# Optimization experiments

Measured on AMD Instinct MI355X. Metric: run time of the kernel, lower is better.

Reference implementation:

```python
import jax, jax.numpy as jnp
import numpy as np

NUM_LAYERS = 3
HIDDEN = 128
EDGE_CH = 4
VOCAB = 100
N_NODES = 100000
N_EDGES = 600000


def setup_inputs() -> dict:
    key = jax.random.key(0)
    ks = jax.random.split(key, 10)
    z = jax.random.randint(ks[0], (N_NODES,), 0, VOCAB)
    edge_index = jax.random.randint(ks[1], (2, N_EDGES), 0, N_NODES)
    edge_attr = jax.random.normal(ks[2], (N_EDGES, EDGE_CH), dtype=jnp.float32)
    batch_vec = jnp.sort(jax.random.randint(ks[3], (N_NODES,), 0, 512))
    s = 1.0 / np.sqrt(HIDDEN)
    emb = jax.random.normal(ks[4], (VOCAB, HIDDEN), dtype=jnp.float32)
    We = jax.random.normal(ks[5], (NUM_LAYERS, EDGE_CH, HIDDEN), dtype=jnp.float32) * 0.5
    be = jnp.zeros((NUM_LAYERS, HIDDEN), dtype=jnp.float32)
    W1 = jax.random.normal(ks[6], (NUM_LAYERS, HIDDEN, HIDDEN), dtype=jnp.float32) * s
    b1 = jnp.zeros((NUM_LAYERS, HIDDEN), dtype=jnp.float32)
    W2 = jax.random.normal(ks[7], (NUM_LAYERS, HIDDEN, HIDDEN), dtype=jnp.float32) * s
    b2 = jnp.zeros((NUM_LAYERS, HIDDEN), dtype=jnp.float32)
    return {"emb": emb, "We": We, "be": be, "W1": W1, "b1": b1,
            "W2": W2, "b2": b2, "edge_attr": edge_attr,
            "z": z, "edge_index": edge_index, "batch_vec": batch_vec}


def reference(emb, We, be, W1, b1, W2, b2, edge_attr, z, edge_index, batch_vec):
    # atom embedding lookup: [N, H]
    x = emb[z]
    src, dst = edge_index[0], edge_index[1]
    n = x.shape[0]
    for l in range(NUM_LAYERS):
        # edge feature projection: [E, H]
        e = edge_attr @ We[l] + be[l]
        # GINE message: relu(x_j + e_ij), gather over src nodes
        m = jax.nn.relu(x[src] + e)
        # scatter-sum aggregation to destination nodes
        agg = jax.ops.segment_sum(m, dst, num_segments=n)
        # (1 + eps) * x + agg, eps = 0, then 2-layer MLP with silu act
        h = x + agg
        x = jax.nn.silu(h @ W1[l] + b1[l]) @ W2[l] + b2[l]
    return (x, batch_vec)
```

## Files before the change

### kernel.cpp

```cpp
#include <hip/hip_runtime.h>
#include <hip/hip_fp16.h>
#include <math.h>

#define N_NODES 100000
#define N_EDGES 600000
#define HIDDEN 128
#define EDGE_CH 4
#define NUM_LAYERS 3
#define MLP_ROWS 64

#define SCAN_BLOCK 256
#define SCAN_GRID ((N_NODES + SCAN_BLOCK - 1) / SCAN_BLOCK)

#define HSTR 132
#define MLP3_TILES ((N_NODES + 127) / 128)
#define MLP3_GRID 256

#define EMB_BLOCKS ((N_NODES * 32) / 256)
#define ZB_BLOCKS  ((N_NODES + 255) / 256)
#define WP_BLOCKS  ((NUM_LAYERS * 2 * HIDDEN * HIDDEN) / 256)

typedef short bf16x8 __attribute__((ext_vector_type(8)));
typedef float f32x4  __attribute__((ext_vector_type(4)));

__device__ inline unsigned short f2bf(float x) {
    unsigned u = __float_as_uint(x);
    return (unsigned short)((u + 0x7fff + ((u >> 16) & 1)) >> 16);
}
__device__ inline float bf2f(unsigned short b) { return __uint_as_float(((unsigned)b) << 16); }

__device__ inline float4 h8tof4(uint2 u) {
    __half2 a = *reinterpret_cast<const __half2*>(&u.x);
    __half2 b = *reinterpret_cast<const __half2*>(&u.y);
    float2 fa = __half22float2(a);
    float2 fb = __half22float2(b);
    return make_float4(fa.x, fa.y, fb.x, fb.y);
}
__device__ inline uint2 f4toh8(float4 v) {
    __half2 a = __floats2half2_rn(v.x, v.y);
    __half2 b = __floats2half2_rn(v.z, v.w);
    uint2 u;
    u.x = *reinterpret_cast<unsigned*>(&a);
    u.y = *reinterpret_cast<unsigned*>(&b);
    return u;
}


__global__ void setup_kernel(const float* __restrict__ emb,
                             const int* __restrict__ z,
                             float* __restrict__ x,
                             __half* __restrict__ xh,
                             int write_xh, int write_x,
                             int* __restrict__ pos,
                             const int* __restrict__ bv,
                             float* __restrict__ out,
                             const float* __restrict__ W1,
                             const float* __restrict__ W2,
                             unsigned short* __restrict__ wt,
                             int do_wprep) {
    int b = blockIdx.x;
    if (b < EMB_BLOCKS) {
        int t = b * 256 + threadIdx.x;
        int node = t >> 5;
        int c4 = t & 31;
        if (node < N_NODES) {
            float4 v = ((const float4*)(emb + (size_t)z[node] * HIDDEN))[c4];
            if (write_x)
                ((float4*)(x + (size_t)node * HIDDEN))[c4] = v;
            if (write_xh)
                ((uint2*)(xh + (size_t)node * HIDDEN))[c4] = f4toh8(v);
        }
    } else if (b < EMB_BLOCKS + ZB_BLOCKS) {
        int i = (b - EMB_BLOCKS) * 256 + threadIdx.x;
        if (i < N_NODES) {
            pos[i] = 0;
            out[i] = (float)bv[i];
        }
    } else if (do_wprep) {
        int idx = (b - EMB_BLOCKS - ZB_BLOCKS) * 256 + threadIdx.x;
        if (idx < NUM_LAYERS * 2 * HIDDEN * HIDDEN) {
            int j    = idx & 7;
            int lane = (idx >> 3) & 63;
            int ks   = (idx >> 9) & 3;
            int nt   = (idx >> 11) & 7;
            int mat  = (idx >> 14) & 1;
            int l    = idx >> 15;
            int n = nt * 16 + (lane & 15);
            int k = ks * 32 + (lane >> 4) * 8 + j;
            const float* W = mat ? W2 : W1;
            wt[idx] = f2bf(W[(size_t)l * HIDDEN * HIDDEN + (size_t)k * HIDDEN + n]);
        }
    }
}


__global__ void embed_init_kernel(const float* __restrict__ emb,
                                  const int* __restrict__ z,
                                  float* __restrict__ x,
                                  float* __restrict__ agg,
                                  int write_agg,
                                  __half* __restrict__ xh,
                                  int write_xh,
                                  int write_x) {
    int t = blockIdx.x * blockDim.x + threadIdx.x;
    int node = t >> 5;
    int c4 = t & 31;
    if (node < N_NODES) {
        float4 v = ((const float4*)(emb + (size_t)z[node] * HIDDEN))[c4];
        if (write_x)
            ((float4*)(x + (size_t)node * HIDDEN))[c4] = v;
        if (write_agg)
            ((float4*)(agg + (size_t)node * HIDDEN))[c4] = v;
        if (write_xh)
            ((uint2*)(xh + (size_t)node * HIDDEN))[c4] = f4toh8(v);
    }
}

__global__ __launch_bounds__(512, 1) void mlp_mfma3_kernel(
        const void* __restrict__ hbuf,
        int h_half,
        const unsigned short* __restrict__ wfrag,
        const float* __restrict__ b1, const float* __restrict__ b2,
        float* __restrict__ x,
        __half* __restrict__ xh,
        int write_x, int write_xh) {
    __shared__ short wlds[2 * 16384];
    __shared__ float tbuf[8 * 16 * HSTR];
    int tid   = threadIdx.x;
    int wave  = tid >> 6;
    int lane  = tid & 63;
    int row16 = lane & 15;
    int quad  = lane >> 4;
    float* myt = tbuf + wave * 16 * HSTR;

    for (int i = tid; i < 4096; i += 512)
        ((float4*)wlds)[i] = ((const float4*)wfrag)[i];
    __syncthreads();

    float bias1[8], bias2[8];
    #pragma unroll
    for (int nt = 0; nt < 8; nt++) {
        bias1[nt] = b1[nt * 16 + row16];
        bias2[nt] = b2[nt * 16 + row16];
    }

    for (int tile = blockIdx.x; tile < MLP3_TILES; tile += gridDim.x) {
        int wnode0 = tile * 128 + wave * 16;
        int mnode  = wnode0 + row16;
        bool valid = (mnode < N_NODES);
        int srcnode = valid ? mnode : 0;

        bf16x8 ahi[4], alo[4];
        if (h_half) {
            const __half* hrow = (const __half*)hbuf + (size_t)srcnode * HIDDEN + quad * 8;
            #pragma unroll
            for (int ks = 0; ks < 4; ks++) {
                float v[8];
                if (valid) {
                    uint4 u = *(const uint4*)(hrow + ks * 32);
                    const __half2* hp = reinterpret_cast<const __half2*>(&u);
                    float2 f0 = __half22float2(hp[0]);
                    float2 f1 = __half22float2(hp[1]);
                    float2 f2 = __half22float2(hp[2]);
                    float2 f3 = __half22float2(hp[3]);
                    v[0]=f0.x; v[1]=f0.y; v[2]=f1.x; v[3]=f1.y;
                    v[4]=f2.x; v[5]=f2.y; v[6]=f3.x; v[7]=f3.y;
                } else {
                    #pragma unroll
                    for (int j = 0; j < 8; j++) v[j] = 0.f;
                }
                bf16x8 hi, lo;
                #pragma unroll
                for (int j = 0; j < 8; j++) {
                    unsigned short hb = f2bf(v[j]);
                    hi[j] = (short)hb;
                    lo[j] = (short)f2bf(v[j] - bf2f(hb));
                }
                ahi[ks] = hi; alo[ks] = lo;
            }
        } else {
            const float* hrow = (const float*)hbuf + (size_t)srcnode * HIDDEN + quad * 8;
            #pragma unroll
            for (int ks = 0; ks < 4; ks++) {
                float v[8];
                *(float4*)(v + 0) = valid ? *(const float4*)(hrow + ks * 32 + 0) : make_float4(0.f,0.f,0.f,0.f);
                *(float4*)(v + 4) = valid ? *(const float4*)(hrow + ks * 32 + 4) : make_float4(0.f,0.f,0.f,0.f);
                bf16x8 hi, lo;
                #pragma unroll
                for (int j = 0; j < 8; j++) {
                    unsigned short hb = f2bf(v[j]);
                    hi[j] = (short)hb;
                    lo[j] = (short)f2bf(v[j] - bf2f(hb));
                }
                ahi[ks] = hi; alo[ks] = lo;
            }
        }

        f32x4 acc[8];
        #pragma unroll
        for (int nt = 0; nt < 8; nt++) acc[nt] = (f32x4){0.f, 0.f, 0.f, 0.f};
        #pragma unroll
        for (int ks = 0; ks < 4; ks++) {
            #pragma unroll
            for (int nt = 0; nt < 8; nt++) {
                bf16x8 Bv = *(const bf16x8*)(wlds + (size_t)((nt * 4 + ks) * 64 + lane) * 8);
                acc[nt] = __builtin_amdgcn_mfma_f32_16x16x32_bf16(ahi[ks], Bv, acc[nt], 0, 0, 0);
                acc[nt] = __builtin_amdgcn_mfma_f32_16x16x32_bf16(alo[ks], Bv, acc[nt], 0, 0, 0);
            }
        }

        #pragma unroll
        for (int nt = 0; nt < 8; nt++) {
            #pragma unroll
            for (int r = 0; r < 4; r++) {
                float v = acc[nt][r] + bias1[nt];
                v = v / (1.f + __expf(-v));
                myt[(quad * 4 + r) * HSTR + nt * 16 + row16] = v;
            }
        }

        #pragma unroll
        for (int ks = 0; ks < 4; ks++) {
            const float* p = myt + row16 * HSTR + ks * 32 + quad * 8;
            float v[8];
            *(float4*)(v + 0) = *(const float4*)(p + 0);
            *(float4*)(v + 4) = *(const float4*)(p + 4);
            bf16x8 hi, lo;
            #pragma unroll
            for (int j = 0; j < 8; j++) {
                unsigned short hb = f2bf(v[j]);
                hi[j] = (short)hb;
                lo[j] = (short)f2bf(v[j] - bf2f(hb));
            }
            ahi[ks] = hi; alo[ks] = lo;
        }

        #pragma unroll
        for (int nt = 0; nt < 8; nt++) acc[nt] = (f32x4){0.f, 0.f, 0.f, 0.f};
        #pragma unroll
        for (int ks = 0; ks < 4; ks++) {
            #pragma unroll
            for (int nt = 0; nt < 8; nt++) {
                bf16x8 Bv = *(const bf16x8*)(wlds + (size_t)(16384 + ((nt * 4 + ks) * 64 + lane) * 8));
                acc[nt] = __builtin_amdgcn_mfma_f32_16x16x32_bf16(ahi[ks], Bv, acc[nt], 0, 0, 0);
                acc[nt] = __builtin_amdgcn_mfma_f32_16x16x32_bf16(alo[ks], Bv, acc[nt], 0, 0, 0);
            }
        }

        #pragma unroll
        for (int nt = 0; nt < 8; nt++) {
            #pragma unroll
            for (int r = 0; r < 4; r++)
                myt[(quad * 4 + r) * HSTR + nt * 16 + row16] = acc[nt][r] + bias2[nt];
        }
        int onode = wnode0 + row16;
        if (onode < N_NODES) {
            const float* prow = myt + row16 * HSTR + quad * 32;
            if (write_x) {
                float* orow = x + (size_t)onode * HIDDEN + quad * 32;
                #pragma unroll
                for (int j = 0; j < 8; j++)
                    *(float4*)(orow + 4 * j) = *(const float4*)(prow + 4 * j);
            }
            if (write_xh) {
                uint2* hrow2 = (uint2*)(xh + (size_t)onode * HIDDEN + quad * 32);
                #pragma unroll
                for (int j = 0; j < 8; j++)
                    hrow2[j] = f4toh8(*(const float4*)(prow + 4 * j));
            }
        }
    }
}

__global__ void mlp_kernel(const float* __restrict__ h,
                           const float* __restrict__ W1, const float* __restrict__ b1,
                           const float* __restrict__ W2, const float* __restrict__ b2,
                           float* __restrict__ x) {
    __shared__ float hs[MLP_ROWS * HIDDEN];
    int rg = threadIdx.x >> 5;
    int c4 = threadIdx.x & 31;
    int node0 = blockIdx.x * MLP_ROWS;

    for (int i = threadIdx.x; i < MLP_ROWS * 32; i += 256) {
        int node = node0 + (i >> 5);
        float4 v = (node < N_NODES)
                 ? ((const float4*)(h + (size_t)node * HIDDEN))[i & 31]
                 : make_float4(0.f, 0.f, 0.f, 0.f);
        ((float4*)hs)[i] = v;
    }
    __syncthreads();

    float4 acc[8];
    {
        float4 bv = ((const float4*)b1)[c4];
        #pragma unroll
        for (int r = 0; r < 8; r++) acc[r] = bv;
    }
    const float* hbase = hs + rg * 8 * HIDDEN;

    for (int k4 = 0; k4 < HIDDEN; k4 += 4) {
        float4 w0 = ((const float4*)(W1 + (size_t)(k4 + 0) * HIDDEN))[c4];
        float4 w1 = ((const float4*)(W1 + (size_t)(k4 + 1) * HIDDEN))[c4];
        float4 w2 = ((const float4*)(W1 + (size_t)(k4 + 2) * HIDDEN))[c4];
        float4 w3 = ((const float4*)(W1 + (size_t)(k4 + 3) * HIDDEN))[c4];
        #pragma unroll
        for (int r = 0; r < 8; r++) {
            float4 hv = *(const float4*)(hbase + r * HIDDEN + k4);
            acc[r].x += hv.x*w0.x + hv.y*w1.x + hv.z*w2.x + hv.w*w3.x;
            acc[r].y += hv.x*w0.y + hv.y*w1.y + hv.z*w2.y + hv.w*w3.y;
            acc[r].z += hv.x*w0.z + hv.y*w1.z + hv.z*w2.z + hv.w*w3.z;
            acc[r].w += hv.x*w0.w + hv.y*w1.w + hv.z*w2.w + hv.w*w3.w;
        }
    }

    __syncthreads();
    #pragma unroll
    for (int r = 0; r < 8; r++) {
        float4 a = acc[r];
        a.x = a.x / (1.f + __expf(-a.x));
        a.y = a.y / (1.f + __expf(-a.y));
        a.z = a.z / (1.f + __expf(-a.z));
        a.w = a.w / (1.f + __expf(-a.w));
        *(float4*)(hs + (rg * 8 + r) * HIDDEN + c4 * 4) = a;
    }
    __syncthreads();

    {
        float4 bv = ((const float4*)b2)[c4];
        #pragma unroll
        for (int r = 0; r < 8; r++) acc[r] = bv;
    }
    for (int k4 = 0; k4 < HIDDEN; k4 += 4) {
        float4 w0 = ((const float4*)(W2 + (size_t)(k4 + 0) * HIDDEN))[c4];
        float4 w1 = ((const float4*)(W2 + (size_t)(k4 + 1) * HIDDEN))[c4];
        float4 w2 = ((const float4*)(W2 + (size_t)(k4 + 2) * HIDDEN))[c4];
        float4 w3 = ((const float4*)(W2 + (size_t)(k4 + 3) * HIDDEN))[c4];
        #pragma unroll
        for (int r = 0; r < 8; r++) {
            float4 hv = *(const float4*)(hbase + r * HIDDEN + k4);
            acc[r].x += hv.x*w0.x + hv.y*w1.x + hv.z*w2.x + hv.w*w3.x;
            acc[r].y += hv.x*w0.y + hv.y*w1.y + hv.z*w2.y + hv.w*w3.y;
            acc[r].z += hv.x*w0.z + hv.y*w1.z + hv.z*w2.z + hv.w*w3.z;
            acc[r].w += hv.x*w0.w + hv.y*w1.w + hv.z*w2.w + hv.w*w3.w;
        }
    }

    #pragma unroll
    for (int r = 0; r < 8; r++) {
        int node = node0 + rg * 8 + r;
        if (node < N_NODES)
            ((float4*)(x + (size_t)node * HIDDEN))[c4] = acc[r];
    }
}

__global__ void batch_out_kernel(const int* __restrict__ bv, float* __restrict__ out) {
    int i = blockIdx.x * blockDim.x + threadIdx.x;
    if (i < N_NODES) out[i] = (float)bv[i];
}


__global__ void zero_kernel(int* __restrict__ p, int n) {
    int i = blockIdx.x * blockDim.x + threadIdx.x;
    if (i < n) p[i] = 0;
}

__global__ void hist_kernel(const int* __restrict__ dst, int* __restrict__ cnt) {
    int e = blockIdx.x * blockDim.x + threadIdx.x;
    if (e < N_EDGES) atomicAdd(&cnt[dst[e]], 1);
}

__global__ void scan_partial_kernel(const int* __restrict__ cnt, int* __restrict__ bsum) {
    __shared__ int s[SCAN_BLOCK];
    int i = blockIdx.x * SCAN_BLOCK + threadIdx.x;
    s[threadIdx.x] = (i < N_NODES) ? cnt[i] : 0;
    __syncthreads();
    for (int off = SCAN_BLOCK / 2; off > 0; off >>= 1) {
        if (threadIdx.x < off) s[threadIdx.x] += s[threadIdx.x + off];
        __syncthreads();
    }
    if (threadIdx.x == 0) bsum[blockIdx.x] = s[0];
}

__global__ void scan_base_kernel(int* __restrict__ bsum) {
    __shared__ int s[512];
    int t = threadIdx.x;
    s[t] = (t < SCAN_GRID) ? bsum[t] : 0;
    __syncthreads();
    for (int off = 1; off < 512; off <<= 1) {
        int v = (t >= off) ? s[t - off] : 0;
        __syncthreads();
        s[t] += v;
        __syncthreads();
    }
    if (t < SCAN_GRID) bsum[t] = (t > 0) ? s[t - 1] : 0;
}

__global__ void scan_final_kernel(int* __restrict__ cnt, const int* __restrict__ bsum) {
    __shared__ int s[SCAN_BLOCK];
    int i = blockIdx.x * SCAN_BLOCK + threadIdx.x;
    int v = (i < N_NODES) ? cnt[i] : 0;
    s[threadIdx.x] = v;
    __syncthreads();
    for (int off = 1; off < SCAN_BLOCK; off <<= 1) {
        int u = (threadIdx.x >= off) ? s[threadIdx.x - off] : 0;
        __syncthreads();
        s[threadIdx.x] += u;
        __syncthreads();
    }
    if (i < N_NODES) cnt[i] = bsum[blockIdx.x] + s[threadIdx.x] - v;
}

__global__ void scatter2_kernel(const int* __restrict__ dst,
                                const int* __restrict__ src,
                                const float* __restrict__ edge_attr,
                                int* __restrict__ pos,
                                int* __restrict__ ssrc,
                                float4* __restrict__ sea) {
    int e = blockIdx.x * blockDim.x + threadIdx.x;
    if (e < N_EDGES) {
        int p = atomicAdd(&pos[dst[e]], 1);
        ssrc[p] = src[e];
        sea[p] = ((const float4*)edge_attr)[e];
    }
}

__global__ void gather2_kernel(const float* __restrict__ x,
                               const int* __restrict__ ssrc,
                               const float4* __restrict__ sea,
                               const int* __restrict__ pos,
                               const float* __restrict__ We_l,
                               const float* __restrict__ be_l,
                               float* __restrict__ h) {
    __shared__ float sWe[EDGE_CH * HIDDEN];
    __shared__ float sbe[HIDDEN];
    for (int i = threadIdx.x; i < EDGE_CH * HIDDEN; i += blockDim.x) sWe[i] = We_l[i];
    if (threadIdx.x < HIDDEN) sbe[threadIdx.x] = be_l[threadIdx.x];
    __syncthreads();

    int t = blockIdx.x * blockDim.x + threadIdx.x;
    int node = t >> 5;
    int c4 = t & 31;
    if (node >= N_NODES) return;

    int start = (node == 0) ? 0 : pos[node - 1];
    int end = pos[node];

    float4 w0 = ((const float4*)sWe)[0 * 32 + c4];
    float4 w1 = ((const float4*)sWe)[1 * 32 + c4];
    float4 w2 = ((const float4*)sWe)[2 * 32 + c4];
    float4 w3 = ((const float4*)sWe)[3 * 32 + c4];
    float4 bb = ((const float4*)sbe)[c4];

    float4 acc = make_float4(0.f, 0.f, 0.f, 0.f);
    int j = start;
    if (j < end) {
        int s0 = ssrc[j];
        float4 ea0 = sea[j];
        for (; j + 1 < end; j++) {
            int s1 = ssrc[j + 1];
            float4 ea1 = sea[j + 1];
            float4 xv = ((const float4*)(x + (size_t)s0 * HIDDEN))[c4];
            float m0 = xv.x + ea0.x*w0.x + ea0.y*w1.x + ea0.z*w2.x + ea0.w*w3.x + bb.x;
            float m1 = xv.y + ea0.x*w0.y + ea0.y*w1.y + ea0.z*w2.y + ea0.w*w3.y + bb.y;
            float m2 = xv.z + ea0.x*w0.z + ea0.y*w1.z + ea0.z*w2.z + ea0.w*w3.z + bb.z;
            float m3 = xv.w + ea0.x*w0.w + ea0.y*w1.w + ea0.z*w2.w + ea0.w*w3.w + bb.w;
            acc.x += fmaxf(m0, 0.f); acc.y += fmaxf(m1, 0.f);
            acc.z += fmaxf(m2, 0.f); acc.w += fmaxf(m3, 0.f);
            s0 = s1; ea0 = ea1;
        }
        float4 xv = ((const float4*)(x + (size_t)s0 * HIDDEN))[c4];
        float m0 = xv.x + ea0.x*w0.x + ea0.y*w1.x + ea0.z*w2.x + ea0.w*w3.x + bb.x;
        float m1 = xv.y + ea0.x*w0.y + ea0.y*w1.y + ea0.z*w2.y + ea0.w*w3.y + bb.y;
        float m2 = xv.z + ea0.x*w0.z + ea0.y*w1.z + ea0.z*w2.z + ea0.w*w3.z + bb.z;
        float m3 = xv.w + ea0.x*w0.w + ea0.y*w1.w + ea0.z*w2.w + ea0.w*w3.w + bb.w;
        acc.x += fmaxf(m0, 0.f); acc.y += fmaxf(m1, 0.f);
        acc.z += fmaxf(m2, 0.f); acc.w += fmaxf(m3, 0.f);
    }
    float4 xi = ((const float4*)(x + (size_t)node * HIDDEN))[c4];
    acc.x += xi.x; acc.y += xi.y; acc.z += xi.z; acc.w += xi.w;
    ((float4*)(h + (size_t)node * HIDDEN))[c4] = acc;
}

__global__ void gather3_kernel(const __half* __restrict__ xh,
                               const int* __restrict__ ssrc,
                               const float4* __restrict__ sea,
                               const int* __restrict__ pos,
                               const float* __restrict__ We_l,
                               const float* __restrict__ be_l,
                               __half* __restrict__ h) {
    __shared__ float sWe[EDGE_CH * HIDDEN];
    __shared__ float sbe[HIDDEN];
    for (int i = threadIdx.x; i < EDGE_CH * HIDDEN; i += blockDim.x) sWe[i] = We_l[i];
    if (threadIdx.x < HIDDEN) sbe[threadIdx.x] = be_l[threadIdx.x];
    __syncthreads();

    int t = blockIdx.x * blockDim.x + threadIdx.x;
    int node = t >> 5;
    int c4 = t & 31;
    if (node >= N_NODES) return;

    int start = (node == 0) ? 0 : pos[node - 1];
    int end = pos[node];

    float4 w0 = ((const float4*)sWe)[0 * 32 + c4];
    float4 w1 = ((const float4*)sWe)[1 * 32 + c4];
    float4 w2 = ((const float4*)sWe)[2 * 32 + c4];
    float4 w3 = ((const float4*)sWe)[3 * 32 + c4];
    float4 bb = ((const float4*)sbe)[c4];

    float4 acc = make_float4(0.f, 0.f, 0.f, 0.f);
    int j = start;
    if (j < end) {
        int s0 = ssrc[j];
        float4 ea0 = sea[j];
        for (; j + 1 < end; j++) {
            int s1 = ssrc[j + 1];
            float4 ea1 = sea[j + 1];
            float4 xv = h8tof4(((const uint2*)(xh + (size_t)s0 * HIDDEN))[c4]);
            float m0 = xv.x + ea0.x*w0.x + ea0.y*w1.x + ea0.z*w2.x + ea0.w*w3.x + bb.x;
            float m1 = xv.y + ea0.x*w0.y + ea0.y*w1.y + ea0.z*w2.y + ea0.w*w3.y + bb.y;
            float m2 = xv.z + ea0.x*w0.z + ea0.y*w1.z + ea0.z*w2.z + ea0.w*w3.z + bb.z;
            float m3 = xv.w + ea0.x*w0.w + ea0.y*w1.w + ea0.z*w2.w + ea0.w*w3.w + bb.w;
            acc.x += fmaxf(m0, 0.f); acc.y += fmaxf(m1, 0.f);
            acc.z += fmaxf(m2, 0.f); acc.w += fmaxf(m3, 0.f);
            s0 = s1; ea0 = ea1;
        }
        float4 xv = h8tof4(((const uint2*)(xh + (size_t)s0 * HIDDEN))[c4]);
        float m0 = xv.x + ea0.x*w0.x + ea0.y*w1.x + ea0.z*w2.x + ea0.w*w3.x + bb.x;
        float m1 = xv.y + ea0.x*w0.y + ea0.y*w1.y + ea0.z*w2.y + ea0.w*w3.y + bb.y;
        float m2 = xv.z + ea0.x*w0.z + ea0.y*w1.z + ea0.z*w2.z + ea0.w*w3.z + bb.z;
        float m3 = xv.w + ea0.x*w0.w + ea0.y*w1.w + ea0.z*w2.w + ea0.w*w3.w + bb.w;
        acc.x += fmaxf(m0, 0.f); acc.y += fmaxf(m1, 0.f);
        acc.z += fmaxf(m2, 0.f); acc.w += fmaxf(m3, 0.f);
    }
    float4 xi = h8tof4(((const uint2*)(xh + (size_t)node * HIDDEN))[c4]);
    acc.x += xi.x; acc.y += xi.y; acc.z += xi.z; acc.w += xi.w;
    ((uint2*)(h + (size_t)node * HIDDEN))[c4] = f4toh8(acc);
}


__global__ void edge_kernel(const float* __restrict__ x,
                            const float* __restrict__ edge_attr,
                            const int* __restrict__ src,
                            const int* __restrict__ dst,
                            const float* __restrict__ We_l,
                            const float* __restrict__ be_l,
                            float* __restrict__ agg) {
    __shared__ float sWe[EDGE_CH * HIDDEN];
    __shared__ float sbe[HIDDEN];
    for (int i = threadIdx.x; i < EDGE_CH * HIDDEN; i += blockDim.x) sWe[i] = We_l[i];
    if (threadIdx.x < HIDDEN) sbe[threadIdx.x] = be_l[threadIdx.x];
    __syncthreads();

    int t = blockIdx.x * blockDim.x + threadIdx.x;
    int e = t >> 5;
    if (e >= N_EDGES) return;
    int c4 = t & 31;

    int s = src[e];
    int d = dst[e];
    float4 ea = ((const float4*)edge_attr)[e];
    float4 w0 = ((const float4*)sWe)[0 * 32 + c4];
    float4 w1 = ((const float4*)sWe)[1 * 32 + c4];
    float4 w2 = ((const float4*)sWe)[2 * 32 + c4];
    float4 w3 = ((const float4*)sWe)[3 * 32 + c4];
    float4 bb = ((const float4*)sbe)[c4];
    float4 xv = ((const float4*)(x + (size_t)s * HIDDEN))[c4];

    float m0 = xv.x + ea.x*w0.x + ea.y*w1.x + ea.z*w2.x + ea.w*w3.x + bb.x;
    float m1 = xv.y + ea.x*w0.y + ea.y*w1.y + ea.z*w2.y + ea.w*w3.y + bb.y;
    float m2 = xv.z + ea.x*w0.z + ea.y*w1.z + ea.z*w2.z + ea.w*w3.z + bb.z;
    float m3 = xv.w + ea.x*w0.w + ea.y*w1.w + ea.z*w2.w + ea.w*w3.w + bb.w;

    float* ap = agg + (size_t)d * HIDDEN + c4 * 4;
    atomicAdd(ap + 0, fmaxf(m0, 0.f));
    atomicAdd(ap + 1, fmaxf(m1, 0.f));
    atomicAdd(ap + 2, fmaxf(m2, 0.f));
    atomicAdd(ap + 3, fmaxf(m3, 0.f));
}


extern "C" void kernel_launch(void* const* d_in, const int* in_sizes, int n_in,
                              void* d_out, int out_size, void* d_ws, size_t ws_size,
                              hipStream_t stream) {
    const float* emb       = (const float*)d_in[0];
    const float* We        = (const float*)d_in[1];
    const float* be        = (const float*)d_in[2];
    const float* W1        = (const float*)d_in[3];
    const float* b1        = (const float*)d_in[4];
    const float* W2        = (const float*)d_in[5];
    const float* b2        = (const float*)d_in[6];
    const float* edge_attr = (const float*)d_in[7];
    const int*   z         = (const int*)d_in[8];
    const int*   ei        = (const int*)d_in[9];
    const int*   bv        = (const int*)d_in[10];

    float* x   = (float*)d_out;
    float* agg = (float*)d_ws;
    const int* src = ei;
    const int* dst = ei + N_EDGES;

    const size_t AGG_BYTES  = (size_t)N_NODES * HIDDEN * sizeof(float);
    const size_t POS_BYTES  = (size_t)N_NODES * sizeof(int);
    const size_t SRC_BYTES  = (size_t)N_EDGES * sizeof(int);
    const size_t EA_BYTES   = (size_t)N_EDGES * 4 * sizeof(float);
    const size_t BSUM_BYTES = ((size_t)SCAN_GRID * sizeof(int) + 15) & ~15;
    const size_t WT_ELEMS   = (size_t)NUM_LAYERS * 2 * HIDDEN * HIDDEN;
    const size_t WT_BYTES   = WT_ELEMS * sizeof(unsigned short);
    const size_t XH_BYTES   = (size_t)N_NODES * HIDDEN * sizeof(__half);

    const size_t OFF_POS  = AGG_BYTES;
    const size_t OFF_SRC  = OFF_POS + POS_BYTES;
    const size_t OFF_EA   = OFF_SRC + SRC_BYTES;
    const size_t OFF_BSUM = OFF_EA + EA_BYTES;
    const size_t OFF_WT   = OFF_BSUM + BSUM_BYTES;
    const size_t OFF_XH   = OFF_WT + WT_BYTES;
    const size_t TOTAL    = OFF_WT + WT_BYTES;
    const size_t TOTAL2   = OFF_XH + XH_BYTES;

    const int MLP_GRID = (N_NODES + MLP_ROWS - 1) / MLP_ROWS;

    if (ws_size >= OFF_BSUM + BSUM_BYTES) {
        int*    pos  = (int*)((char*)d_ws + OFF_POS);
        int*    ssrc = (int*)((char*)d_ws + OFF_SRC);
        float4* sea  = (float4*)((char*)d_ws + OFF_EA);
        int*    bsum = (int*)((char*)d_ws + OFF_BSUM);
        const bool mfma  = (ws_size >= TOTAL);
        const bool halfx = (ws_size >= TOTAL2);
        unsigned short* wt = (unsigned short*)((char*)d_ws + OFF_WT);
        __half* xh = (__half*)((char*)d_ws + OFF_XH);

        setup_kernel<<<EMB_BLOCKS + ZB_BLOCKS + WP_BLOCKS, 256, 0, stream>>>(
            emb, z, x, xh, halfx ? 1 : 0, halfx ? 0 : 1,
            pos, bv, x + (size_t)N_NODES * HIDDEN,
            W1, W2, wt, mfma ? 1 : 0);
        hist_kernel<<<(N_EDGES + 255) / 256, 256, 0, stream>>>(dst, pos);
        scan_partial_kernel<<<SCAN_GRID, SCAN_BLOCK, 0, stream>>>(pos, bsum);
        scan_base_kernel<<<1, 512, 0, stream>>>(bsum);
        scan_final_kernel<<<SCAN_GRID, SCAN_BLOCK, 0, stream>>>(pos, bsum);
        scatter2_kernel<<<(N_EDGES + 255) / 256, 256, 0, stream>>>(dst, src, edge_attr, pos, ssrc, sea);

        for (int l = 0; l < NUM_LAYERS; l++) {
            if (halfx) {
                gather3_kernel<<<(N_NODES * 32 + 255) / 256, 256, 0, stream>>>(
                    xh, ssrc, sea, pos,
                    We + (size_t)l * EDGE_CH * HIDDEN, be + (size_t)l * HIDDEN,
                    (__half*)agg);
            } else {
                gather2_kernel<<<(N_NODES * 32 + 255) / 256, 256, 0, stream>>>(
                    x, ssrc, sea, pos,
                    We + (size_t)l * EDGE_CH * HIDDEN, be + (size_t)l * HIDDEN, agg);
            }
            if (mfma) {
                int wx  = (!halfx || l == NUM_LAYERS - 1) ? 1 : 0;
                int wxh = (halfx && l < NUM_LAYERS - 1) ? 1 : 0;
                mlp_mfma3_kernel<<<MLP3_GRID, 512, 0, stream>>>(
                    (const void*)agg, halfx ? 1 : 0,
                    wt + (size_t)(l * 2) * HIDDEN * HIDDEN,
                    b1 + (size_t)l * HIDDEN, b2 + (size_t)l * HIDDEN, x, xh, wx, wxh);
            } else {
                mlp_kernel<<<MLP_GRID, 256, 0, stream>>>(
                    agg,
                    W1 + (size_t)l * HIDDEN * HIDDEN, b1 + (size_t)l * HIDDEN,
                    W2 + (size_t)l * HIDDEN * HIDDEN, b2 + (size_t)l * HIDDEN, x);
            }
        }
    } else {
        embed_init_kernel<<<(N_NODES * 32) / 256, 256, 0, stream>>>(
            emb, z, x, agg, 1, (__half*)nullptr, 0, 1);
        for (int l = 0; l < NUM_LAYERS; l++) {
            edge_kernel<<<(N_EDGES * 32) / 256, 256, 0, stream>>>(
                x, edge_attr, src, dst,
                We + (size_t)l * EDGE_CH * HIDDEN, be + (size_t)l * HIDDEN, agg);
            mlp_kernel<<<MLP_GRID, 256, 0, stream>>>(
                agg,
                W1 + (size_t)l * HIDDEN * HIDDEN, b1 + (size_t)l * HIDDEN,
                W2 + (size_t)l * HIDDEN * HIDDEN, b2 + (size_t)l * HIDDEN, x);
        }
        batch_out_kernel<<<(N_NODES + 255) / 256, 256, 0, stream>>>(bv, x + (size_t)N_NODES * HIDDEN);
    }
}
```

Baseline: 416.8 us.

## Double MLP block to 16 waves and halve per-wave LDS staging buffer

The fused MLP kernel now launches 1024 threads (16 waves) per block, each handling 256 nodes per tile. The hidden activation is staged through LDS in two 64-column halves, so each wave's transpose buffer shrinks from a 132-float stride to 68. The half-precision output is written via an LDS half buffer with 16-byte stores. The aim is to fit more waves per CU within the LDS budget and hide MFMA and memory latency, at the cost of extra staging passes and added register pressure under the 1024-thread launch bound.

```diff
diff --git a/kernel.cpp b/kernel.cpp
--- a/kernel.cpp
+++ b/kernel.cpp
@@ -12,9 +12,9 @@
 #define SCAN_BLOCK 256
 #define SCAN_GRID ((N_NODES + SCAN_BLOCK - 1) / SCAN_BLOCK)
 
-#define HSTR 132
-#define MLP3_TILES ((N_NODES + 127) / 128)
-#define MLP3_GRID 256
+#define TSTR 68
+#define MLP5_TILES ((N_NODES + 255) / 256)
+#define MLP5_GRID 256
 
 #define EMB_BLOCKS ((N_NODES * 32) / 256)
 #define ZB_BLOCKS  ((N_NODES + 255) / 256)
@@ -116,7 +116,7 @@
     }
 }
 
-__global__ __launch_bounds__(512, 1) void mlp_mfma3_kernel(
+__global__ __launch_bounds__(1024, 1) void mlp_mfma5_kernel(
         const void* __restrict__ hbuf,
         int h_half,
         const unsigned short* __restrict__ wfrag,
@@ -125,15 +125,15 @@
         __half* __restrict__ xh,
         int write_x, int write_xh) {
     __shared__ short wlds[2 * 16384];
-    __shared__ float tbuf[8 * 16 * HSTR];
+    __shared__ float tbuf[16 * 16 * TSTR];
     int tid   = threadIdx.x;
     int wave  = tid >> 6;
     int lane  = tid & 63;
     int row16 = lane & 15;
     int quad  = lane >> 4;
-    float* myt = tbuf + wave * 16 * HSTR;
-
-    for (int i = tid; i < 4096; i += 512)
+    float* myt = tbuf + wave * 16 * TSTR;
+
+    for (int i = tid; i < 4096; i += 1024)
         ((float4*)wlds)[i] = ((const float4*)wfrag)[i];
     __syncthreads();
 
@@ -144,8 +144,8 @@
         bias2[nt] = b2[nt * 16 + row16];
     }
 
-    for (int tile = blockIdx.x; tile < MLP3_TILES; tile += gridDim.x) {
-        int wnode0 = tile * 128 + wave * 16;
+    for (int tile = blockIdx.x; tile < MLP5_TILES; tile += gridDim.x) {
+        int wnode0 = tile * 256 + wave * 16;
         int mnode  = wnode0 + row16;
         bool valid = (mnode < N_NODES);
         int srcnode = valid ? mnode : 0;
@@ -196,77 +196,99 @@
             }
         }
 
-        f32x4 acc[8];
+        f32x4 acc1[8];
         #pragma unroll
-        for (int nt = 0; nt < 8; nt++) acc[nt] = (f32x4){0.f, 0.f, 0.f, 0.f};
+        for (int nt = 0; nt < 8; nt++) acc1[nt] = (f32x4){0.f, 0.f, 0.f, 0.f};
         #pragma unroll
         for (int ks = 0; ks < 4; ks++) {
             #pragma unroll
             for (int nt = 0; nt < 8; nt++) {
                 bf16x8 Bv = *(const bf16x8*)(wlds + (size_t)((nt * 4 + ks) * 64 + lane) * 8);
-                acc[nt] = __builtin_amdgcn_mfma_f32_16x16x32_bf16(ahi[ks], Bv, acc[nt], 0, 0, 0);
-                acc[nt] = __builtin_amdgcn_mfma_f32_16x16x32_bf16(alo[ks], Bv, acc[nt], 0, 0, 0);
-            }
-        }
-
+                acc1[nt] = __builtin_amdgcn_mfma_f32_16x16x32_bf16(ahi[ks], Bv, acc1[nt], 0, 0, 0);
+                acc1[nt] = __builtin_amdgcn_mfma_f32_16x16x32_bf16(alo[ks], Bv, acc1[nt], 0, 0, 0);
+            }
+        }
+
+        f32x4 acc2[8];
         #pragma unroll
-        for (int nt = 0; nt < 8; nt++) {
+        for (int nt = 0; nt < 8; nt++) acc2[nt] = (f32x4){0.f, 0.f, 0.f, 0.f};
+
+        #pragma unroll
+        for (int p = 0; p < 2; p++) {
             #pragma unroll
-            for (int r = 0; r < 4; r++) {
-                float v = acc[nt][r] + bias1[nt];
-                v = v / (1.f + __expf(-v));
-                myt[(quad * 4 + r) * HSTR + nt * 16 + row16] = v;
-            }
-        }
-
-        #pragma unroll
-        for (int ks = 0; ks < 4; ks++) {
-            const float* p = myt + row16 * HSTR + ks * 32 + quad * 8;
-            float v[8];
-            *(float4*)(v + 0) = *(const float4*)(p + 0);
-            *(float4*)(v + 4) = *(const float4*)(p + 4);
-            bf16x8 hi, lo;
+            for (int l4 = 0; l4 < 4; l4++) {
+                int nt = p * 4 + l4;
+                #pragma unroll
+                for (int r = 0; r < 4; r++) {
+                    float v = acc1[nt][r] + bias1[nt];
+                    v = v / (1.f + __expf(-v));
+                    myt[(quad * 4 + r) * TSTR + l4 * 16 + row16] = v;
+                }
+            }
+
+            bf16x8 a2hi[2], a2lo[2];
             #pragma unroll
-            for (int j = 0; j < 8; j++) {
-                unsigned short hb = f2bf(v[j]);
-                hi[j] = (short)hb;
-                lo[j] = (short)f2bf(v[j] - bf2f(hb));
-            }
-            ahi[ks] = hi; alo[ks] = lo;
-        }
-
-        #pragma unroll
-        for (int nt = 0; nt < 8; nt++) acc[nt] = (f32x4){0.f, 0.f, 0.f, 0.f};
-        #pragma unroll
-        for (int ks = 0; ks < 4; ks++) {
+            for (int kk = 0; kk < 2; kk++) {
+                const float* pp = myt + row16 * TSTR + kk * 32 + quad * 8;
+                float v[8];
+                *(float4*)(v + 0) = *(const float4*)(pp + 0);
+                *(float4*)(v + 4) = *(const float4*)(pp + 4);
+                bf16x8 hi, lo;
+                #pragma unroll
+                for (int j = 0; j < 8; j++) {
+                    unsigned short hb = f2bf(v[j]);
+                    hi[j] = (short)hb;
+                    lo[j] = (short)f2bf(v[j] - bf2f(hb));
+                }
+                a2hi[kk] = hi; a2lo[kk] = lo;
+            }
+
+            #pragma unroll
+            for (int kk = 0; kk < 2; kk++) {
+                int ks = p * 2 + kk;
+                #pragma unroll
+                for (int nt = 0; nt < 8; nt++) {
+                    bf16x8 Bv = *(const bf16x8*)(wlds + (size_t)(16384 + ((nt * 4 + ks) * 64 + lane) * 8));
+                    acc2[nt] = __builtin_amdgcn_mfma_f32_16x16x32_bf16(a2hi[kk], Bv, acc2[nt], 0, 0, 0);
+                    acc2[nt] = __builtin_amdgcn_mfma_f32_16x16x32_bf16(a2lo[kk], Bv, acc2[nt], 0, 0, 0);
+                }
+            }
+        }
+
+        int onode = wnode0 + row16;
+        if (write_xh) {
+            __half* hmyt = (__half*)myt;
             #pragma unroll
             for (int nt = 0; nt < 8; nt++) {
-                bf16x8 Bv = *(const bf16x8*)(wlds + (size_t)(16384 + ((nt * 4 + ks) * 64 + lane) * 8));
-                acc[nt] = __builtin_amdgcn_mfma_f32_16x16x32_bf16(ahi[ks], Bv, acc[nt], 0, 0, 0);
-                acc[nt] = __builtin_amdgcn_mfma_f32_16x16x32_bf16(alo[ks], Bv, acc[nt], 0, 0, 0);
-            }
-        }
-
-        #pragma unroll
-        for (int nt = 0; nt < 8; nt++) {
+                #pragma unroll
+                for (int r = 0; r < 4; r++)
+                    hmyt[(quad * 4 + r) * 136 + nt * 16 + row16] =
+                        __float2half_rn(acc2[nt][r] + bias2[nt]);
+            }
+            if (onode < N_NODES) {
+                const uint4* pr = (const uint4*)(hmyt + row16 * 136 + quad * 32);
+                uint4* orow = (uint4*)(xh + (size_t)onode * HIDDEN + quad * 32);
+                #pragma unroll
+                for (int j = 0; j < 4; j++) orow[j] = pr[j];
+            }
+        }
+        if (write_x) {
             #pragma unroll
-            for (int r = 0; r < 4; r++)
-                myt[(quad * 4 + r) * HSTR + nt * 16 + row16] = acc[nt][r] + bias2[nt];
-        }
-        int onode = wnode0 + row16;
-        if (onode < N_NODES) {
-            const float* prow = myt + row16 * HSTR + quad * 32;
-            if (write_x) {
-                float* orow = x + (size_t)onode * HIDDEN + quad * 32;
+            for (int p = 0; p < 2; p++) {
                 #pragma unroll
-                for (int j = 0; j < 8; j++)
-                    *(float4*)(orow + 4 * j) = *(const float4*)(prow + 4 * j);
-            }
-            if (write_xh) {
-                uint2* hrow2 = (uint2*)(xh + (size_t)onode * HIDDEN + quad * 32);
-                #pragma unroll
-                for (int j = 0; j < 8; j++)
-                    hrow2[j] = f4toh8(*(const float4*)(prow + 4 * j));
+                for (int l4 = 0; l4 < 4; l4++) {
+                    int nt = p * 4 + l4;
+                    #pragma unroll
+                    for (int r = 0; r < 4; r++)
+                        myt[(quad * 4 + r) * TSTR + l4 * 16 + row16] = acc2[nt][r] + bias2[nt];
+                }
+                if (onode < N_NODES) {
+                    const float* prow = myt + row16 * TSTR + quad * 16;
+                    float* orow = x + (size_t)onode * HIDDEN + p * 64 + quad * 16;
+                    #pragma unroll
+                    for (int j = 0; j < 4; j++)
+                        *(float4*)(orow + 4 * j) = *(const float4*)(prow + 4 * j);
+                }
             }
         }
     }
@@ -654,7 +676,7 @@
             if (mfma) {
                 int wx  = (!halfx || l == NUM_LAYERS - 1) ? 1 : 0;
                 int wxh = (halfx && l < NUM_LAYERS - 1) ? 1 : 0;
-                mlp_mfma3_kernel<<<MLP3_GRID, 512, 0, stream>>>(
+                mlp_mfma5_kernel<<<MLP5_GRID, 1024, 0, stream>>>(
                     (const void*)agg, halfx ? 1 : 0,
                     wt + (size_t)(l * 2) * HIDDEN * HIDDEN,
                     b1 + (size_t)l * HIDDEN, b2 + (size_t)l * HIDDEN, x, xh, wx, wxh);
```

Measured after the change: 406.7 us. 1.02x faster.
